# Performance work log

Hardware: AMD Instinct MI355X
Metric: run time of the kernel (lower is better)

The kernel has to match this reference:

```python
import jax, jax.numpy as jnp
import numpy as np

B, N, NT, ET = 16, 38, 9, 4
NE = N * (N - 1) // 2          # 703 edge-generation steps
R = N + NE                     # repeat_num = 741 masked subgraphs
H = D = 128                    # nhid / nout
L = 12                         # num_flow_layer
EDIM = ET - 1                  # 3 relation types used by RGCN
EPS = 1e-5
TEMP = 0.1                     # straight-through argmax temperature


def _st_dis(x, w1, b1, w2, b2):
    # MLP -> logits -> straight-through one-hot(argmax)
    h = jnp.tanh(x @ w1.T + b1)
    logits = h @ w2.T + b2
    soft = jax.nn.softmax(logits / TEMP, axis=-1)
    hard = jax.nn.one_hot(jnp.argmax(logits, axis=-1), logits.shape[-1], dtype=logits.dtype)
    return soft + jax.lax.stop_gradient(hard - soft)


def _one_hot_add(inputs, shift):
    # (inputs + shift) mod vocab in one-hot space == circular conv via FFT
    out = jnp.fft.ifft(jnp.fft.fft(inputs, axis=-1) * jnp.fft.fft(shift, axis=-1), axis=-1)
    return jnp.real(out).astype(inputs.dtype)


def _gconv(x, adj, w):
    # x: (b, n, f_in), adj: (b, e, n, n), w: (e*f_out, f_in)
    b, n, _ = x.shape
    s = (x @ w.T).reshape(b, n, EDIM, -1)            # (b, n, e, f_out)
    return jnp.einsum('beij,bjeo->bio', adj, s)      # aggregate over relations


def _rgcn(x, adj, emb_w, gc1_w, gc2_w, gc3_w):
    h = x @ emb_w.T
    h = jax.nn.relu(_gconv(h, adj, gc1_w))
    h = jax.nn.relu(_gconv(h, adj, gc2_w))
    return _gconv(h, adj, gc3_w)                     # no relu on last layer


def setup_inputs():
    key = jax.random.key(0)
    ks = jax.random.split(key, 16)
    s = 0.1
    iu, ju = np.triu_indices(N, k=1)                 # canonical edge order (703, 2)
    return {
        'x': jax.random.uniform(ks[0], (B, N, NT), dtype=jnp.float32),
        'adj': jax.random.uniform(ks[1], (B, ET, N, N), dtype=jnp.float32),
        'x_deq': jax.random.normal(ks[2], (B, N, NT), dtype=jnp.float32),
        'adj_deq': jax.random.normal(ks[3], (B, NE, ET), dtype=jnp.float32),
        'mask_node': jax.random.uniform(ks[4], (R, N)) < 0.5,
        'mask_edge': jax.random.uniform(ks[5], (R, N, N)) < 0.5,
        'index_select_edge': jnp.asarray(np.stack([iu, ju], 1), dtype=jnp.int32),
        'emb_w': jax.random.normal(ks[6], (NT, NT), jnp.float32) * s,
        'gc1_w': jax.random.normal(ks[7], (EDIM * H, NT), jnp.float32) * s,
        'gc2_w': jax.random.normal(ks[8], (EDIM * H, H), jnp.float32) * s,
        'gc3_w': jax.random.normal(ks[9], (EDIM * D, H), jnp.float32) * s,
        'bn_gamma': jnp.ones((D,), jnp.float32),
        'bn_beta': jnp.zeros((D,), jnp.float32),
        'node_w1': jax.random.normal(ks[10], (L, H, D), jnp.float32) * s,
        'node_b1': jnp.zeros((L, H), jnp.float32),
        'node_w2': jax.random.normal(ks[11], (L, NT, H), jnp.float32) * s,
        'node_b2': jnp.zeros((L, NT), jnp.float32),
        'edge_w1': jax.random.normal(ks[12], (L, H, 3 * D), jnp.float32) * s,
        'edge_b1': jnp.zeros((L, H), jnp.float32),
        'edge_w2': jax.random.normal(ks[13], (L, ET, H), jnp.float32) * s,
        'edge_b2': jnp.zeros((L, ET), jnp.float32),
    }


def reference(x, adj, x_deq, adj_deq, mask_node, mask_edge, index_select_edge,
              emb_w, gc1_w, gc2_w, gc3_w, bn_gamma, bn_beta,
              node_w1, node_b1, node_w2, node_b2,
              edge_w1, edge_b1, edge_w2, edge_b2):
    adj3 = adj[:, :EDIM]                                              # (B,3,N,N)
    xr = jnp.where(mask_node[None, :, :, None], x[:, None], 0.0)      # (B,R,N,NT)
    ar = jnp.where(mask_edge[None, :, None], adj3[:, None], 0.0)      # (B,R,3,N,N)
    xr = xr.reshape(B * R, N, NT)
    ar = ar.reshape(B * R, EDIM, N, N)
    node_emb = _rgcn(xr, ar, emb_w, gc1_w, gc2_w, gc3_w)              # (B*R,N,D)
    # BatchNorm1d over channels (training-mode batch statistics, biased var)
    m = node_emb.mean(axis=(0, 1))
    v = node_emb.var(axis=(0, 1))
    node_emb = (node_emb - m) * jax.lax.rsqrt(v + EPS) * bn_gamma + bn_beta
    node_emb = node_emb.reshape(B, R, N, D)
    graph_emb = node_emb.sum(axis=2)                                  # (B,R,D)
    graph_emb_node = graph_emb[:, :N]                                 # (B,N,D)
    graph_emb_edge = graph_emb[:, N:, None]                           # (B,NE,1,D)
    all_node_emb_edge = node_emb[:, N:]                               # (B,NE,N,D)
    idx = jnp.broadcast_to(index_select_edge[None, :, :, None].astype(jnp.int32), (B, NE, 2, D))
    sel = jnp.take_along_axis(all_node_emb_edge, idx, axis=2)         # (B,NE,2,D)
    graph_node_emb_edge = jnp.concatenate([sel, graph_emb_edge], axis=2).reshape(B, NE, 3 * D)
    xd, ad = x_deq, adj_deq
    for i in range(L):
        nt = _st_dis(graph_emb_node, node_w1[i], node_b1[i], node_w2[i], node_b2[i]).astype(x.dtype)
        xd = _one_hot_add(xd, nt)
        et = _st_dis(graph_node_emb_edge, edge_w1[i], edge_b1[i], edge_w2[i], edge_b2[i]).astype(adj.dtype)
        ad = _one_hot_add(ad, et)
    return (xd, ad)
```

## Files before the change

### kernel.cpp

```cpp
#include <hip/hip_runtime.h>

#define B_   16
#define N_   38
#define NT_  9
#define ET_  4
#define NE_  703
#define R_   741
#define L_   12
#define BR_  11856

__global__ __launch_bounds__(128) void k_sx(const float* __restrict__ x,
                                            const float* __restrict__ emb_w,
                                            const float* __restrict__ gc1_w,
                                            float* __restrict__ sx)
{
  int bn = blockIdx.x;
  int t  = threadIdx.x;
  __shared__ float xr[NT_];
  __shared__ float hx[NT_];
  if (t < NT_) xr[t] = x[bn*NT_ + t];
  __syncthreads();
  if (t < NT_) {
    float s = 0.f;
    #pragma unroll
    for (int u = 0; u < NT_; ++u) s += xr[u] * emb_w[t*NT_ + u];
    hx[t] = s;
  }
  __syncthreads();
  for (int eo = t; eo < 384; eo += 128) {
    float s = 0.f;
    #pragma unroll
    for (int u = 0; u < NT_; ++u) s += hx[u] * gc1_w[eo*NT_ + u];
    sx[bn*384 + eo] = s;
  }
}

__global__ __launch_bounds__(128) void k_wt(const float* __restrict__ gc2_w,
                                            const float* __restrict__ gc3_w,
                                            float* __restrict__ Wt)
{
  int blk   = blockIdx.x;
  int which = blk / 384;
  int rem   = blk - which*384;
  int e     = rem >> 7;
  int k     = rem & 127;
  int o     = threadIdx.x;
  const float* src = which ? gc3_w : gc2_w;
  Wt[(((which*3 + e) << 7) + k)*128 + o] = src[((e << 7) + o)*128 + k];
}

__global__ __launch_bounds__(128) void k_wt2(const float* __restrict__ node_w1,
                                             const float* __restrict__ edge_w1,
                                             float* __restrict__ w1t_e,
                                             float* __restrict__ w1t_n)
{
  int blk = blockIdx.x;
  int o   = threadIdx.x;
  if (blk < 12*384) {
    int l = blk / 384, kk = blk - l*384;
    w1t_e[blk*128 + o] = edge_w1[(l*128 + o)*384 + kk];
  } else {
    int row = blk - 12*384;
    int l = row >> 7, k = row & 127;
    w1t_n[row*128 + o] = node_w1[(l*128 + o)*128 + k];
  }
}

__device__ __forceinline__ void fma4(float4& d, float a, const float4& s) {
  d.x += a*s.x; d.y += a*s.y; d.z += a*s.z; d.w += a*s.w;
}

__device__ __forceinline__ void ldA(const float* __restrict__ adj,
                                    const int* __restrict__ mask_edge,
                                    int b, int r, int e, int tid,
                                    float av[5], float a1v[2])
{
  #pragma unroll
  for (int t = 0; t < 5; ++t) {
    int m = tid + (t << 8);
    float v = 0.f;
    if (m < 1216) {
      int j = m >> 5, slot = m & 31;
      int i = (slot >> 2) + ((slot & 3) << 3);
      int   msk = mask_edge[(r*N_ + i)*N_ + j];
      float a   = adj[((b*ET_ + e)*N_ + i)*N_ + j];
      v = msk ? a : 0.f;
    }
    av[t] = v;
  }
  #pragma unroll
  for (int t = 0; t < 2; ++t) {
    int m = tid + (t << 8);
    float v = 0.f;
    if (m < 304) {
      int j = m >> 3;
      int i = (m & 7) + 32;
      if (i < N_) {
        int   msk = mask_edge[(r*N_ + i)*N_ + j];
        float a   = adj[((b*ET_ + e)*N_ + i)*N_ + j];
        v = msk ? a : 0.f;
      }
    }
    a1v[t] = v;
  }
}

__device__ __forceinline__ void stA(float* __restrict__ A4e,
                                    float* __restrict__ A1e, int tid,
                                    const float av[5], const float a1v[2])
{
  #pragma unroll
  for (int t = 0; t < 5; ++t) {
    int m = tid + (t << 8);
    if (m < 1216) A4e[m] = av[t];
  }
  #pragma unroll
  for (int t = 0; t < 2; ++t) {
    int m = tid + (t << 8);
    if (m < 304) A1e[m] = a1v[t];
  }
}

__device__ __forceinline__ void eacc_m(const float* __restrict__ A4e,
                                       const float* __restrict__ A1e,
                                       const float* __restrict__ S_l,
                                       int p, int c,
                                       const int* __restrict__ mn,
                                       float4 d[5])
{
  #pragma unroll 2
  for (int j = 0; j < 38; ++j) {
    if (!mn[j]) continue;
    float4 s4 = *(const float4*)&S_l[(j << 7) + (c << 2)];
    float4 a4 = *(const float4*)&A4e[(j << 5) + (p << 2)];
    float  a1 = A1e[(j << 3) + p];
    fma4(d[0], a4.x, s4); fma4(d[1], a4.y, s4); fma4(d[2], a4.z, s4);
    fma4(d[3], a4.w, s4); fma4(d[4], a1,   s4);
  }
}

__device__ __forceinline__ void eacc_u(const float* __restrict__ A4e,
                                       const float* __restrict__ A1e,
                                       const float* __restrict__ S_l,
                                       int p, int c,
                                       float4 d[5])
{
  #pragma unroll 4
  for (int j = 0; j < 38; ++j) {
    float4 s4 = *(const float4*)&S_l[(j << 7) + (c << 2)];
    float4 a4 = *(const float4*)&A4e[(j << 5) + (p << 2)];
    float  a1 = A1e[(j << 3) + p];
    fma4(d[0], a4.x, s4); fma4(d[1], a4.y, s4); fma4(d[2], a4.z, s4);
    fma4(d[3], a4.w, s4); fma4(d[4], a1,   s4);
  }
}

__device__ __forceinline__ void gemm_fused(const float* __restrict__ H_l,
                                           const float* __restrict__ Wb,
                                           int p, int c, float4 g[3][5])
{
  #pragma unroll
  for (int e = 0; e < 3; ++e)
    #pragma unroll
    for (int q = 0; q < 5; ++q) { g[e][q].x = 0.f; g[e][q].y = 0.f; g[e][q].z = 0.f; g[e][q].w = 0.f; }
  #pragma unroll 1
  for (int k0 = 0; k0 < 128; k0 += 4) {
    float4 h0 = *(const float4*)&H_l[((p+ 0) << 7) + k0];
    float4 h1 = *(const float4*)&H_l[((p+ 8) << 7) + k0];
    float4 h2 = *(const float4*)&H_l[((p+16) << 7) + k0];
    float4 h3 = *(const float4*)&H_l[((p+24) << 7) + k0];
    float4 h4 = *(const float4*)&H_l[((p+32) << 7) + k0];
    #pragma unroll
    for (int e = 0; e < 3; ++e) {
      const float* We = &Wb[(e << 14) + (k0 << 7) + (c << 2)];
      float4 w0 = *(const float4*)&We[  0];
      float4 w1 = *(const float4*)&We[128];
      float4 w2 = *(const float4*)&We[256];
      float4 w3 = *(const float4*)&We[384];
      fma4(g[e][0], h0.x, w0); fma4(g[e][0], h0.y, w1); fma4(g[e][0], h0.z, w2); fma4(g[e][0], h0.w, w3);
      fma4(g[e][1], h1.x, w0); fma4(g[e][1], h1.y, w1); fma4(g[e][1], h1.z, w2); fma4(g[e][1], h1.w, w3);
      fma4(g[e][2], h2.x, w0); fma4(g[e][2], h2.y, w1); fma4(g[e][2], h2.z, w2); fma4(g[e][2], h2.w, w3);
      fma4(g[e][3], h3.x, w0); fma4(g[e][3], h3.y, w1); fma4(g[e][3], h3.z, w2); fma4(g[e][3], h3.w, w3);
      fma4(g[e][4], h4.x, w0); fma4(g[e][4], h4.y, w1); fma4(g[e][4], h4.z, w2); fma4(g[e][4], h4.w, w3);
    }
  }
}

__device__ __forceinline__ void relu_store(float* __restrict__ H_l, int p, int c,
                                           const float4 d[5])
{
  #pragma unroll
  for (int q = 0; q < 5; ++q) {
    float4 t;
    t.x = fmaxf(d[q].x, 0.f); t.y = fmaxf(d[q].y, 0.f);
    t.z = fmaxf(d[q].z, 0.f); t.w = fmaxf(d[q].w, 0.f);
    *(float4*)&H_l[((p + (q << 3)) << 7) + (c << 2)] = t;
  }
}

__global__ __launch_bounds__(256) void k_rgcn(
    const float* __restrict__ adj, const int* __restrict__ mask_node,
    const int* __restrict__ mask_edge, const int* __restrict__ isel,
    const float* __restrict__ sx, const float* __restrict__ Wt,
    float* __restrict__ sumE, float* __restrict__ sumSq,
    float* __restrict__ selw)
{
  const int br  = blockIdx.x;
  const int b   = br / R_;
  const int r   = br - b*R_;
  const int tid = threadIdx.x;
  const int c   = tid & 31;
  const int p   = tid >> 5;

  __shared__ __align__(16) float A4_l[3*1216];
  __shared__ __align__(16) float A1_l[3*304];
  __shared__ __align__(16) float SH_l[40*128];
  __shared__ int mn_l[40];

  if (tid < 40) mn_l[tid] = (tid < 38) ? mask_node[r*N_ + tid] : 0;

  float av[5], a1v[2];
  ldA(adj, mask_edge, b, r, 0, tid, av, a1v);
  __syncthreads();

  float4 d[5];
  #pragma unroll
  for (int q = 0; q < 5; ++q) { d[q].x = d[q].y = d[q].z = d[q].w = 0.f; }

  for (int e = 0; e < 3; ++e) {
    for (int idx = tid; idx < 40*32; idx += 256) {
      int j = idx >> 5, q4 = idx & 31;
      float4 v; v.x = v.y = v.z = v.w = 0.f;
      if (j < N_ && mn_l[j]) v = *(const float4*)&sx[(b*N_ + j)*384 + (e << 7) + (q4 << 2)];
      *(float4*)&SH_l[(j << 7) + (q4 << 2)] = v;
    }
    stA(&A4_l[e*1216], &A1_l[e*304], tid, av, a1v);
    __syncthreads();
    if (e < 2) ldA(adj, mask_edge, b, r, e+1, tid, av, a1v);
    eacc_m(&A4_l[e*1216], &A1_l[e*304], SH_l, p, c, mn_l, d);
    __syncthreads();
  }
  relu_store(SH_l, p, c, d);
  __syncthreads();

  for (int gv = 0; gv < 2; ++gv) {
    float4 g[3][5];
    gemm_fused(SH_l, &Wt[gv*49152], p, c, g);
    #pragma unroll
    for (int q = 0; q < 5; ++q) { d[q].x = d[q].y = d[q].z = d[q].w = 0.f; }
    #pragma unroll
    for (int e = 0; e < 3; ++e) {
      __syncthreads();
      #pragma unroll
      for (int q = 0; q < 5; ++q)
        *(float4*)&SH_l[((p + (q << 3)) << 7) + (c << 2)] = g[e][q];
      __syncthreads();
      eacc_u(&A4_l[e*1216], &A1_l[e*304], SH_l, p, c, d);
    }
    if (gv == 0) {
      __syncthreads();
      relu_store(SH_l, p, c, d);
      __syncthreads();
    }
  }
  __syncthreads();

  {
    float4 sA, sB;
    sA.x = d[0].x+d[1].x+d[2].x+d[3].x+d[4].x;
    sA.y = d[0].y+d[1].y+d[2].y+d[3].y+d[4].y;
    sA.z = d[0].z+d[1].z+d[2].z+d[3].z+d[4].z;
    sA.w = d[0].w+d[1].w+d[2].w+d[3].w+d[4].w;
    sB.x = d[0].x*d[0].x+d[1].x*d[1].x+d[2].x*d[2].x+d[3].x*d[3].x+d[4].x*d[4].x;
    sB.y = d[0].y*d[0].y+d[1].y*d[1].y+d[2].y*d[2].y+d[3].y*d[3].y+d[4].y*d[4].y;
    sB.z = d[0].z*d[0].z+d[1].z*d[1].z+d[2].z*d[2].z+d[3].z*d[3].z+d[4].z*d[4].z;
    sB.w = d[0].w*d[0].w+d[1].w*d[1].w+d[2].w*d[2].w+d[3].w*d[3].w+d[4].w*d[4].w;
    *(float4*)&SH_l[( p      << 7) + (c << 2)] = sA;
    *(float4*)&SH_l[((8 + p) << 7) + (c << 2)] = sB;
  }
  __syncthreads();
  {
    int o = tid & 127, half = tid >> 7;
    float t = 0.f;
    #pragma unroll
    for (int pp = 0; pp < 8; ++pp) t += SH_l[(((half << 3) + pp) << 7) + o];
    if (half == 0) sumE [br*128 + o] = t;
    else           sumSq[br*128 + o] = t;
  }
  if (r >= N_) {
    int k  = r - N_;
    int iu = isel[2*k], ju = isel[2*k+1];
    if (p == (iu & 7)) {
      int mu = iu >> 3;
      float4 v = d[0];
      if (mu == 1) v = d[1]; else if (mu == 2) v = d[2];
      else if (mu == 3) v = d[3]; else if (mu == 4) v = d[4];
      *(float4*)&selw[(((b*NE_ + k)*2 + 0) << 7) + (c << 2)] = v;
    }
    if (p == (ju & 7)) {
      int mu = ju >> 3;
      float4 v = d[0];
      if (mu == 1) v = d[1]; else if (mu == 2) v = d[2];
      else if (mu == 3) v = d[3]; else if (mu == 4) v = d[4];
      *(float4*)&selw[(((b*NE_ + k)*2 + 1) << 7) + (c << 2)] = v;
    }
  }
}

__global__ __launch_bounds__(256) void k_zero(int* __restrict__ Pn,
                                              int* __restrict__ Pe)
{
  int i = blockIdx.x*256 + threadIdx.x;
  if (i < B_*N_)   Pn[i] = 0;
  if (i < B_*NE_)  Pe[i] = 0;
}

__global__ __launch_bounds__(256) void k_bn1(const float* __restrict__ sumE,
                                             const float* __restrict__ sumSq,
                                             double* __restrict__ part)
{
  int g = blockIdx.x;
  int t = threadIdx.x;
  int o = t & 127, h = t >> 7;
  int lo = g*47;
  int hi = lo + 47; if (hi > BR_) hi = BR_;
  double a1 = 0.0, a2 = 0.0;
  for (int i = lo + h; i < hi; i += 2) {
    a1 += (double)sumE [i*128 + o];
    a2 += (double)sumSq[i*128 + o];
  }
  __shared__ double sh1[256], sh2[256];
  sh1[t] = a1; sh2[t] = a2;
  __syncthreads();
  if (h == 0) {
    part[g*128 + o]           = sh1[o] + sh1[128 + o];
    part[256*128 + g*128 + o] = sh2[o] + sh2[128 + o];
  }
}

__global__ __launch_bounds__(128) void k_bn2(const double* __restrict__ part,
                                             const float* __restrict__ gamma,
                                             const float* __restrict__ beta,
                                             float* __restrict__ bnsc,
                                             float* __restrict__ bnsh)
{
  int o = threadIdx.x;
  double s1 = 0.0, s2 = 0.0;
  for (int g = 0; g < 256; ++g) {
    s1 += part[g*128 + o];
    s2 += part[256*128 + g*128 + o];
  }
  double cnt = (double)BR_ * 38.0;
  double m   = s1 / cnt;
  double var = s2 / cnt - m*m;
  double rs  = 1.0 / sqrt(var + 1e-5);
  double sc  = (double)gamma[o] * rs;
  bnsc[o] = (float)sc;
  bnsh[o] = beta[o] - (float)(m * sc);
}

__global__ __launch_bounds__(128) void k_node_par(
    const float* __restrict__ sumE, const float* __restrict__ bnsc,
    const float* __restrict__ bnsh,
    const float* __restrict__ w1t_n, const float* __restrict__ b1,
    const float* __restrict__ w2, const float* __restrict__ b2,
    int* __restrict__ Pn)
{
  int blk = blockIdx.x;
  int l   = blk / (B_*N_);
  int bn  = blk - l*(B_*N_);
  int b   = bn / N_;
  int o   = threadIdx.x;
  __shared__ __align__(16) float xv[128];
  __shared__ __align__(16) float hb[128];
  __shared__ float lg[NT_];
  int br = b*R_ + (bn - b*N_);
  xv[o] = sumE[br*128 + o]*bnsc[o] + 38.f*bnsh[o];
  __syncthreads();
  const float* wb = &w1t_n[l << 14];
  float s = b1[l*128 + o];
  #pragma unroll 2
  for (int k = 0; k < 128; k += 4) {
    float4 x4 = *(const float4*)&xv[k];
    s += wb[((k+0) << 7) + o]*x4.x + wb[((k+1) << 7) + o]*x4.y
       + wb[((k+2) << 7) + o]*x4.z + wb[((k+3) << 7) + o]*x4.w;
  }
  hb[o] = tanhf(s);
  __syncthreads();
  if (o < NT_) {
    const float* w2r = &w2[(l*NT_ + o)*128];
    float s2 = b2[l*NT_ + o];
    for (int k = 0; k < 128; ++k) s2 += w2r[k]*hb[k];
    lg[o] = s2;
  }
  __syncthreads();
  if (o == 0) {
    int best = 0; float bv = lg[0];
    #pragma unroll
    for (int cc = 1; cc < NT_; ++cc) if (lg[cc] > bv) { bv = lg[cc]; best = cc; }
    atomicAdd(&Pn[bn], best);
  }
}

__global__ __launch_bounds__(128) void k_edge_par(
    const float* __restrict__ sumE, const float* __restrict__ selw,
    const float* __restrict__ bnsc, const float* __restrict__ bnsh,
    const float* __restrict__ w1t_e, const float* __restrict__ b1,
    const float* __restrict__ w2, const float* __restrict__ b2,
    int* __restrict__ Pe)
{
  int blk = blockIdx.x;
  int l = blk / NE_;
  int k = blk - l*NE_;
  int t = threadIdx.x;
  int c = t & 31, p = t >> 5;
  __shared__ __align__(16) float xv[16][384];
  __shared__ __align__(16) float hb[16][132];
  __shared__ float lg[16][4];

  for (int idx = t; idx < 16*128; idx += 128) {
    int b = idx >> 7, oo = idx & 127;
    float sc = bnsc[oo], sh = bnsh[oo];
    int base = ((b*NE_ + k)*2)*128;
    xv[b][oo]       = selw[base + oo]      *sc + sh;
    xv[b][128 + oo] = selw[base + 128 + oo]*sc + sh;
    xv[b][256 + oo] = sumE[(b*R_ + N_ + k)*128 + oo]*sc + 38.f*sh;
  }
  __syncthreads();

  float4 acc[4];
  {
    float4 bb4 = *(const float4*)&b1[(l << 7) + (c << 2)];
    acc[0] = bb4; acc[1] = bb4; acc[2] = bb4; acc[3] = bb4;
  }
  const float* wl = &w1t_e[(l*384) << 7];
  #pragma unroll 2
  for (int kk = 0; kk < 384; kk += 4) {
    const float* wk = wl + (kk << 7) + (c << 2);
    float4 w0 = *(const float4*)&wk[  0];
    float4 w1 = *(const float4*)&wk[128];
    float4 w2v= *(const float4*)&wk[256];
    float4 w3 = *(const float4*)&wk[384];
    #pragma unroll
    for (int m = 0; m < 4; ++m) {
      float4 x = *(const float4*)&xv[p + (m << 2)][kk];
      fma4(acc[m], x.x, w0); fma4(acc[m], x.y, w1);
      fma4(acc[m], x.z, w2v); fma4(acc[m], x.w, w3);
    }
  }
  #pragma unroll
  for (int m = 0; m < 4; ++m) {
    float4 h;
    h.x = tanhf(acc[m].x); h.y = tanhf(acc[m].y);
    h.z = tanhf(acc[m].z); h.w = tanhf(acc[m].w);
    *(float4*)&hb[p + (m << 2)][c << 2] = h;
  }
  __syncthreads();
  if (t < 64) {
    int m = t >> 2, c2 = t & 3;
    const float* w2r = &w2[(l*ET_ + c2)*128];
    float s2 = b2[l*ET_ + c2];
    for (int kk = 0; kk < 128; ++kk) s2 += w2r[kk]*hb[m][kk];
    lg[m][c2] = s2;
  }
  __syncthreads();
  if (t < 16) {
    int best = 0; float bv = lg[t][0];
    #pragma unroll
    for (int cc = 1; cc < ET_; ++cc) if (lg[t][cc] > bv) { bv = lg[t][cc]; best = cc; }
    atomicAdd(&Pe[t*NE_ + k], best);
  }
}

__global__ __launch_bounds__(64) void k_gather(
    const int* __restrict__ Pn, const int* __restrict__ Pe,
    const float* __restrict__ x_deq, const float* __restrict__ adj_deq,
    float* __restrict__ out)
{
  int blk = blockIdx.x;
  int t   = threadIdx.x;
  if (blk < B_*N_) {
    if (t < NT_) {
      int P = Pn[blk] % NT_;
      int src = t - P; if (src < 0) src += NT_;
      out[blk*NT_ + t] = x_deq[blk*NT_ + src];
    }
  } else {
    int k = blk - B_*N_;
    int m = t >> 2, c2 = t & 3;
    int P = Pe[m*NE_ + k] & 3;
    int src = c2 - P; if (src < 0) src += ET_;
    out[B_*N_*NT_ + (m*NE_ + k)*ET_ + c2] = adj_deq[(m*NE_ + k)*ET_ + src];
  }
}

extern "C" void kernel_launch(void* const* d_in, const int* in_sizes, int n_in,
                              void* d_out, int out_size, void* d_ws, size_t ws_size,
                              hipStream_t stream)
{
  (void)in_sizes; (void)n_in; (void)out_size; (void)ws_size;

  const float* x         = (const float*)d_in[0];
  const float* adj       = (const float*)d_in[1];
  const float* x_deq     = (const float*)d_in[2];
  const float* adj_deq   = (const float*)d_in[3];
  const int*   mask_node = (const int*)d_in[4];
  const int*   mask_edge = (const int*)d_in[5];
  const int*   isel      = (const int*)d_in[6];
  const float* emb_w     = (const float*)d_in[7];
  const float* gc1_w     = (const float*)d_in[8];
  const float* gc2_w     = (const float*)d_in[9];
  const float* gc3_w     = (const float*)d_in[10];
  const float* bn_gamma  = (const float*)d_in[11];
  const float* bn_beta   = (const float*)d_in[12];
  const float* node_w1   = (const float*)d_in[13];
  const float* node_b1   = (const float*)d_in[14];
  const float* node_w2   = (const float*)d_in[15];
  const float* node_b2   = (const float*)d_in[16];
  const float* edge_w1   = (const float*)d_in[17];
  const float* edge_b1   = (const float*)d_in[18];
  const float* edge_w2   = (const float*)d_in[19];
  const float* edge_b2   = (const float*)d_in[20];

  float* out_f = (float*)d_out;

  float*  wsf   = (float*)d_ws;
  float*  sx    = wsf;
  float*  sumE  = sx    + 233472;
  float*  sumSq = sumE  + 1517568;
  float*  selw  = sumSq + 1517568;
  float*  bnsc  = selw  + 2879488;
  float*  bnsh  = bnsc  + 128;
  double* part  = (double*)(bnsh + 128);
  float*  Wt    = (float*)part;
  float*  w1t_e = sumSq;
  float*  w1t_n = sumSq + 589824;
  int*    Pn    = (int*)sx;
  int*    Pe    = Pn + B_*N_;

  k_wt      <<<768,           128, 0, stream>>>(gc2_w, gc3_w, Wt);
  k_sx      <<<B_*N_,         128, 0, stream>>>(x, emb_w, gc1_w, sx);
  k_rgcn    <<<BR_,           256, 0, stream>>>(adj, mask_node, mask_edge, isel,
                                                sx, Wt, sumE, sumSq, selw);
  k_zero    <<<(B_*NE_ + 255)/256, 256, 0, stream>>>(Pn, Pe);
  k_bn1     <<<256,           256, 0, stream>>>(sumE, sumSq, part);
  k_bn2     <<<1,             128, 0, stream>>>(part, bn_gamma, bn_beta, bnsc, bnsh);
  k_wt2     <<<12*384+12*128, 128, 0, stream>>>(node_w1, edge_w1, w1t_e, w1t_n);
  k_node_par<<<L_*B_*N_,      128, 0, stream>>>(sumE, bnsc, bnsh, w1t_n, node_b1,
                                                node_w2, node_b2, Pn);
  k_edge_par<<<L_*NE_,        128, 0, stream>>>(sumE, selw, bnsc, bnsh, w1t_e,
                                                edge_b1, edge_w2, edge_b2, Pe);
  k_gather  <<<B_*N_ + NE_,    64, 0, stream>>>(Pn, Pe, x_deq, adj_deq, out_f);
}
```

Measured before the change: 2.091 ms.

## Shrink adjacency LDS to two buffers and reload relations from global

Keeps only two relation slices of the masked adjacency in shared memory instead of three. The missing slice is re-read from global memory and re-staged between the later graph-conv passes, with the relation processing order rearranged so the reload overlaps compute. The node mask becomes a 64-bit register bitmask instead of a shared int array. The aim is a smaller LDS footprint so more blocks can be resident, at the cost of extra global reloads of the adjacency and mask data.

```diff
diff --git a/kernel.cpp b/kernel.cpp
--- a/kernel.cpp
+++ b/kernel.cpp
@@ -125,12 +125,12 @@
                                        const float* __restrict__ A1e,
                                        const float* __restrict__ S_l,
                                        int p, int c,
-                                       const int* __restrict__ mn,
+                                       unsigned long long mb,
                                        float4 d[5])
 {
   #pragma unroll 2
   for (int j = 0; j < 38; ++j) {
-    if (!mn[j]) continue;
+    if (!((mb >> j) & 1ull)) continue;
     float4 s4 = *(const float4*)&S_l[(j << 7) + (c << 2)];
     float4 a4 = *(const float4*)&A4e[(j << 5) + (p << 2)];
     float  a1 = A1e[(j << 3) + p];
@@ -198,6 +198,14 @@
   }
 }
 
+__device__ __forceinline__ void store_S(float* __restrict__ SH, int p, int c,
+                                        const float4 g5[5])
+{
+  #pragma unroll
+  for (int q = 0; q < 5; ++q)
+    *(float4*)&SH[((p + (q << 3)) << 7) + (c << 2)] = g5[q];
+}
+
 __global__ __launch_bounds__(256) void k_rgcn(
     const float* __restrict__ adj, const int* __restrict__ mask_node,
     const int* __restrict__ mask_edge, const int* __restrict__ isel,
@@ -212,56 +220,84 @@
   const int c   = tid & 31;
   const int p   = tid >> 5;
 
-  __shared__ __align__(16) float A4_l[3*1216];
-  __shared__ __align__(16) float A1_l[3*304];
+  __shared__ __align__(16) float A4_l[2*1216];
+  __shared__ __align__(16) float A1_l[2*304];
   __shared__ __align__(16) float SH_l[40*128];
-  __shared__ int mn_l[40];
-
-  if (tid < 40) mn_l[tid] = (tid < 38) ? mask_node[r*N_ + tid] : 0;
-
+  __shared__ unsigned int mnb_l[2];
+
+  if (tid < 2) mnb_l[tid] = 0u;
   float av[5], a1v[2];
   ldA(adj, mask_edge, b, r, 0, tid, av, a1v);
   __syncthreads();
+  if (tid < 38 && mask_node[r*N_ + tid]) atomicOr(&mnb_l[tid >> 5], 1u << (tid & 31));
+  __syncthreads();
+  const unsigned long long mb = (unsigned long long)mnb_l[0]
+                              | ((unsigned long long)mnb_l[1] << 32);
 
   float4 d[5];
   #pragma unroll
   for (int q = 0; q < 5; ++q) { d[q].x = d[q].y = d[q].z = d[q].w = 0.f; }
 
   for (int e = 0; e < 3; ++e) {
+    int buf = (e == 1) ? 1 : 0;
     for (int idx = tid; idx < 40*32; idx += 256) {
       int j = idx >> 5, q4 = idx & 31;
       float4 v; v.x = v.y = v.z = v.w = 0.f;
-      if (j < N_ && mn_l[j]) v = *(const float4*)&sx[(b*N_ + j)*384 + (e << 7) + (q4 << 2)];
+      if ((mb >> j) & 1ull) v = *(const float4*)&sx[(b*N_ + j)*384 + (e << 7) + (q4 << 2)];
       *(float4*)&SH_l[(j << 7) + (q4 << 2)] = v;
     }
-    stA(&A4_l[e*1216], &A1_l[e*304], tid, av, a1v);
+    stA(&A4_l[buf*1216], &A1_l[buf*304], tid, av, a1v);
     __syncthreads();
     if (e < 2) ldA(adj, mask_edge, b, r, e+1, tid, av, a1v);
-    eacc_m(&A4_l[e*1216], &A1_l[e*304], SH_l, p, c, mn_l, d);
+    eacc_m(&A4_l[buf*1216], &A1_l[buf*304], SH_l, p, c, mb, d);
     __syncthreads();
   }
   relu_store(SH_l, p, c, d);
   __syncthreads();
 
-  for (int gv = 0; gv < 2; ++gv) {
+  {
     float4 g[3][5];
-    gemm_fused(SH_l, &Wt[gv*49152], p, c, g);
+    gemm_fused(SH_l, &Wt[0], p, c, g);
     #pragma unroll
     for (int q = 0; q < 5; ++q) { d[q].x = d[q].y = d[q].z = d[q].w = 0.f; }
-    #pragma unroll
-    for (int e = 0; e < 3; ++e) {
-      __syncthreads();
-      #pragma unroll
-      for (int q = 0; q < 5; ++q)
-        *(float4*)&SH_l[((p + (q << 3)) << 7) + (c << 2)] = g[e][q];
-      __syncthreads();
-      eacc_u(&A4_l[e*1216], &A1_l[e*304], SH_l, p, c, d);
-    }
-    if (gv == 0) {
-      __syncthreads();
-      relu_store(SH_l, p, c, d);
-      __syncthreads();
-    }
+    __syncthreads();
+    store_S(SH_l, p, c, g[1]);
+    __syncthreads();
+    ldA(adj, mask_edge, b, r, 0, tid, av, a1v);
+    eacc_u(&A4_l[1216], &A1_l[304], SH_l, p, c, d);
+    __syncthreads();
+    store_S(SH_l, p, c, g[2]);
+    __syncthreads();
+    eacc_u(&A4_l[0], &A1_l[0], SH_l, p, c, d);
+    __syncthreads();
+    store_S(SH_l, p, c, g[0]);
+    stA(&A4_l[1216], &A1_l[304], tid, av, a1v);
+    __syncthreads();
+    eacc_u(&A4_l[1216], &A1_l[304], SH_l, p, c, d);
+  }
+  __syncthreads();
+  relu_store(SH_l, p, c, d);
+  __syncthreads();
+
+  {
+    float4 g[3][5];
+    gemm_fused(SH_l, &Wt[49152], p, c, g);
+    #pragma unroll
+    for (int q = 0; q < 5; ++q) { d[q].x = d[q].y = d[q].z = d[q].w = 0.f; }
+    __syncthreads();
+    store_S(SH_l, p, c, g[0]);
+    __syncthreads();
+    ldA(adj, mask_edge, b, r, 1, tid, av, a1v);
+    eacc_u(&A4_l[1216], &A1_l[304], SH_l, p, c, d);
+    __syncthreads();
+    store_S(SH_l, p, c, g[2]);
+    __syncthreads();
+    eacc_u(&A4_l[0], &A1_l[0], SH_l, p, c, d);
+    __syncthreads();
+    store_S(SH_l, p, c, g[1]);
+    stA(&A4_l[1216], &A1_l[304], tid, av, a1v);
+    __syncthreads();
+    eacc_u(&A4_l[1216], &A1_l[304], SH_l, p, c, d);
   }
   __syncthreads();
 
```

Result: slower. 2.239 ms (+7.1%).
